# Optimization experiments

Measured on AMD Instinct MI355X. Metric: run time of the kernel, lower is better.

## Reference

```python
import jax, jax.numpy as jnp
import numpy as np

B, S, E, H = 4, 2048, 1024, 16
D = E // H  # key_size


def setup_inputs() -> dict:
    key = jax.random.key(0)
    ks = jax.random.split(key, 6)
    s = 1.0 / np.sqrt(E)
    return {
        "X": jax.random.normal(ks[0], (B, S, E), dtype=jnp.float32),
        "Wq": jax.random.uniform(ks[1], (E, E), jnp.float32, -s, s),
        "Wk": jax.random.uniform(ks[2], (E, E), jnp.float32, -s, s),
        "Wv": jax.random.uniform(ks[3], (E, E), jnp.float32, -s, s),
        "Wo": jax.random.uniform(ks[4], (E, E), jnp.float32, -s, s),
        "bo": jax.random.uniform(ks[5], (E,), jnp.float32, -s, s),
    }


def reference(X, Wq, Wk, Wv, Wo, bo):
    # Linear layers: y = x @ W^T (torch convention), no bias for q/k/v
    def split(x):  # [B,S,E] -> [B,H,S,D]
        return x.reshape(B, S, H, D).transpose(0, 2, 1, 3)

    q = split(X @ Wq.T)
    k = split(X @ Wk.T)
    v = split(X @ Wv.T)
    scale = jnp.asarray(np.sqrt(D), dtype=X.dtype)
    scores = jnp.einsum("bhqd,bhkd->bhqk", q, k) / scale
    probs = jax.nn.softmax(scores, axis=-1)
    ctx = jnp.einsum("bhqk,bhkd->bhqd", probs, v)
    out = ctx.transpose(0, 2, 1, 3).reshape(B, S, E)
    return out @ Wo.T + bo
```

## Files before the change

### kernel.cpp

```cpp
#include <hip/hip_runtime.h>
#include <hip/hip_bf16.h>

typedef short bf16x8 __attribute__((ext_vector_type(8)));
typedef float f32x4  __attribute__((ext_vector_type(4)));

__device__ __forceinline__ short f2bf(float f) {
    union { float f; unsigned u; } x; x.f = f;
    unsigned r = x.u + 0x7fffu + ((x.u >> 16) & 1u);
    return (short)(r >> 16);
}

__device__ __forceinline__ unsigned rbits(float f) {
    union { float f; unsigned u; } x; x.f = f;
    return x.u + 0x8000u;
}
__device__ __forceinline__ int pack2(float a, float b) {
    return (int)__builtin_amdgcn_perm(rbits(b), rbits(a), 0x07060302u);
}

__device__ __forceinline__ f32x4 mfma32k(bf16x8 a, bf16x8 b, f32x4 c) {
    return __builtin_amdgcn_mfma_f32_16x16x32_bf16(a, b, c, 0, 0, 0);
}

#define GLDS16(g, l)                                                            \
    __builtin_amdgcn_global_load_lds(                                           \
        (const __attribute__((address_space(1))) void*)(g),                     \
        (__attribute__((address_space(3))) void*)(l), 16, 0, 0)

static constexpr int Bb = 4, Ss = 2048, Ee = 1024, Hh = 16, Dd = 64;
static constexpr int Mrows = Bb * Ss;
static constexpr float CL2 = 0.1803368801111204f;

__global__ void cvt_all(const float* __restrict__ X,  const float* __restrict__ Wq,
                        const float* __restrict__ Wk, const float* __restrict__ Wv,
                        const float* __restrict__ Wo,
                        short* __restrict__ Xb, short* __restrict__ Wqk,
                        short* __restrict__ Wvb, short* __restrict__ Wob) {
    int bid = blockIdx.x;
    const float* src; short* dst; int off; float scale = 1.0f;
    if (bid < 8192) {
        src = X; dst = Xb; off = bid * 1024;
    } else {
        int wsel = (bid - 8192) >> 10;
        off = ((bid - 8192) & 1023) * 1024;
        if      (wsel == 0) { src = Wq; dst = Wqk;                scale = CL2; }
        else if (wsel == 1) { src = Wk; dst = Wqk + Ee * Ee; }
        else if (wsel == 2) { src = Wv; dst = Wvb; }
        else                { src = Wo; dst = Wob; }
    }
    int i = off + threadIdx.x * 4;
    float4 v = *(const float4*)(src + i);
    short4 o;
    o.x = f2bf(v.x * scale); o.y = f2bf(v.y * scale);
    o.z = f2bf(v.z * scale); o.w = f2bf(v.w * scale);
    *(short4*)(dst + i) = o;
}

__global__ __launch_bounds__(256, 3)
void gemm_fused(const short* __restrict__ A0, const short* __restrict__ B0,
                short* __restrict__ C0,
                const short* __restrict__ A1, const short* __restrict__ B1,
                short* __restrict__ C1, int split) {
    __shared__ __align__(16) short sA[128 * 32];
    __shared__ __align__(16) short sB[128 * 32];
    const int t = threadIdx.x, w = t >> 6, l = t & 63;
    const int lane16 = l & 15, quad = l >> 4;
    const int wm = (w >> 1) * 64, wn = (w & 1) * 64;

    int bid = blockIdx.x;
    const short *A, *Bm; short* C;
    int bm, bn, ldc; bool perm;
    if (bid < split) {
        bm = bid & 63; bn = bid >> 6;
        A = A0; Bm = B0; C = C0; ldc = 2048; perm = false;
    } else {
        int id = bid - split;
        bm = id & 7; bn = id >> 3;
        A = A1; Bm = B1; C = C1; ldc = 8192; perm = true;
    }

    f32x4 acc[4][4] = {};
    const short* Ab  = A  + (size_t)bm * 128 * 1024;
    const short* Bbp = Bm + (size_t)bn * 128 * 1024;
    const int s0 = w * 64 + l;
    const int ldsOff = (w * 64) * 8;

    for (int k0 = 0; k0 < 1024; k0 += 32) {
#pragma unroll
        for (int p = 0; p < 2; ++p) {
            int s = p * 256 + s0;
            int row = s >> 2, cs = s & 3;
            GLDS16(Ab + (size_t)row * 1024 + k0 + cs * 8, sA + p * 2048 + ldsOff);
            GLDS16(Bbp + (size_t)row * 1024 + k0 + cs * 8, sB + p * 2048 + ldsOff);
        }
        __syncthreads();
        bf16x8 af[4], bfr[4];
#pragma unroll
        for (int i = 0; i < 4; ++i) {
            af[i]  = *(const bf16x8*)(sA + (wm + i * 16 + lane16) * 32 + quad * 8);
            bfr[i] = *(const bf16x8*)(sB + (wn + i * 16 + lane16) * 32 + quad * 8);
        }
#pragma unroll
        for (int i = 0; i < 4; ++i)
#pragma unroll
            for (int j = 0; j < 4; ++j)
                acc[i][j] = mfma32k(af[i], bfr[j], acc[i][j]);
        __syncthreads();
    }

    const int sEven = (lane16 >> 2) * 8 + (lane16 & 3);
#pragma unroll
    for (int i = 0; i < 4; ++i)
#pragma unroll
        for (int j = 0; j < 4; ++j) {
            int row = bm * 128 + wm + i * 16 + quad * 4;
            int col = bn * 128 + wn + j * 16 + lane16;
            if (perm) col = (col & ~31) | (sEven + (j & 1) * 4);
#pragma unroll
            for (int r = 0; r < 4; ++r)
                C[(size_t)(row + r) * ldc + col] = f2bf(acc[i][j][r]);
        }
}

__global__ __launch_bounds__(256, 3)
void gemm_out(const short* __restrict__ A, const short* __restrict__ Bm,
              float* __restrict__ C, const float* __restrict__ bias) {
    __shared__ __align__(16) short sA[128 * 32];
    __shared__ __align__(16) short sB[128 * 32];
    const int t = threadIdx.x, w = t >> 6, l = t & 63;
    const int lane16 = l & 15, quad = l >> 4;
    const int wm = (w >> 1) * 64, wn = (w & 1) * 64;
    const int bm = blockIdx.x, bn = blockIdx.y;

    f32x4 acc[4][4] = {};
    const short* Ab  = A  + (size_t)bm * 128 * 1024;
    const short* Bbp = Bm + (size_t)bn * 128 * 1024;
    const int s0 = w * 64 + l;
    const int ldsOff = (w * 64) * 8;

    for (int k0 = 0; k0 < 1024; k0 += 32) {
#pragma unroll
        for (int p = 0; p < 2; ++p) {
            int s = p * 256 + s0;
            int row = s >> 2, cs = s & 3;
            GLDS16(Ab + (size_t)row * 1024 + k0 + cs * 8, sA + p * 2048 + ldsOff);
            GLDS16(Bbp + (size_t)row * 1024 + k0 + cs * 8, sB + p * 2048 + ldsOff);
        }
        __syncthreads();
        bf16x8 af[4], bfr[4];
#pragma unroll
        for (int i = 0; i < 4; ++i) {
            af[i]  = *(const bf16x8*)(sA + (wm + i * 16 + lane16) * 32 + quad * 8);
            bfr[i] = *(const bf16x8*)(sB + (wn + i * 16 + lane16) * 32 + quad * 8);
        }
#pragma unroll
        for (int i = 0; i < 4; ++i)
#pragma unroll
            for (int j = 0; j < 4; ++j)
                acc[i][j] = mfma32k(af[i], bfr[j], acc[i][j]);
        __syncthreads();
    }

#pragma unroll
    for (int i = 0; i < 4; ++i)
#pragma unroll
        for (int j = 0; j < 4; ++j) {
            int row = bm * 128 + wm + i * 16 + quad * 4;
            int col = bn * 128 + wn + j * 16 + lane16;
            float bv = bias[col];
#pragma unroll
            for (int r = 0; r < 4; ++r)
                C[(size_t)(row + r) * 1024 + col] = acc[i][j][r] + bv;
        }
}

__global__ __launch_bounds__(256, 4)
void attn_kernel(const short* __restrict__ QK, const short* __restrict__ VT,
                 short* __restrict__ CTX) {
    __shared__ __align__(16) short sK[8192];
    __shared__ __align__(16) short sV[8192];
    const int t = threadIdx.x, w = t >> 6, l = t & 63;
    const int lane16 = l & 15, quad = l >> 4;
    const int bh = blockIdx.x, qt = blockIdx.y;
    const int b = bh >> 4, h = bh & 15;

    const int qx8 = (quad ^ ((lane16 >> 1) & 3)) * 8;

    const short* Qb = QK + ((size_t)(b * 2048 + qt * 128)) * 2048 + h * 64;
    const short* Vb = VT + ((size_t)(h * 64)) * 8192 + (size_t)b * 2048;
    const int ldsOff = (w * 64) * 8;

    int off_kq[4], off_v[4];
#pragma unroll
    for (int p = 0; p < 4; ++p) {
        int c = p * 256 + t;
        int sw = ((c & 3) ^ ((c >> 3) & 3)) * 8;
        off_kq[p] = ((c >> 2) & 127) * 2048 + (c >> 9) * 32 + sw;
        off_v[p]  = ((c >> 2) & 63) * 8192 + (c >> 8) * 32 + sw;
    }

#pragma unroll
    for (int p = 0; p < 4; ++p)
        GLDS16(Qb + off_kq[p], sK + p * 2048 + ldsOff);
    __syncthreads();
    bf16x8 qf[2][2];
#pragma unroll
    for (int mt = 0; mt < 2; ++mt)
#pragma unroll
        for (int ks = 0; ks < 2; ++ks)
            qf[mt][ks] = *(const bf16x8*)(sK + ks * 4096 + (w * 32 + mt * 16 + lane16) * 32 + qx8);
    __syncthreads();

    const short one = (short)0x3F80;
    const bf16x8 ONE8 = {one, one, one, one, one, one, one, one};
    f32x4 lacc[2] = {};
    f32x4 o[2][4] = {};

    const short* kptr = QK + ((size_t)(b * 2048)) * 2048 + 1024 + h * 64;
    const short* vptr = Vb;

    auto QKB = [&](int a, f32x4 (&sc)[2][2]) {
        __builtin_amdgcn_s_setprio(1);
#pragma unroll
        for (int sub = 0; sub < 2; ++sub) {
            int nt = a * 2 + sub;
            bf16x8 kf0 = *(const bf16x8*)(sK + (nt * 16 + lane16) * 32 + qx8);
            bf16x8 kf1 = *(const bf16x8*)(sK + 4096 + (nt * 16 + lane16) * 32 + qx8);
#pragma unroll
            for (int mt = 0; mt < 2; ++mt) {
                f32x4 z = {};
                z = mfma32k(kf0, qf[mt][0], z);
                z = mfma32k(kf1, qf[mt][1], z);
                sc[mt][sub] = z;
            }
        }
        __builtin_amdgcn_s_setprio(0);
    };
    auto PVB = [&](int a, f32x4 (&sc)[2][2]) {
        bf16x8 pf[2];
#pragma unroll
        for (int mt = 0; mt < 2; ++mt) {
            union { int i[4]; bf16x8 v; } u;
#pragma unroll
            for (int sub = 0; sub < 2; ++sub) {
                f32x4 e;
#pragma unroll
                for (int r = 0; r < 4; ++r)
                    e[r] = __builtin_amdgcn_exp2f(sc[mt][sub][r]);
                u.i[sub * 2]     = pack2(e[0], e[1]);
                u.i[sub * 2 + 1] = pack2(e[2], e[3]);
            }
            pf[mt] = u.v;
        }
        __builtin_amdgcn_s_setprio(1);
#pragma unroll
        for (int mt = 0; mt < 2; ++mt)
            lacc[mt] = mfma32k(pf[mt], ONE8, lacc[mt]);
#pragma unroll
        for (int dt = 0; dt < 4; ++dt) {
            bf16x8 vf = *(const bf16x8*)(sV + a * 2048 + (dt * 16 + lane16) * 32 + qx8);
#pragma unroll
            for (int mt = 0; mt < 2; ++mt)
                o[mt][dt] = mfma32k(pf[mt], vf, o[mt][dt]);
        }
        __builtin_amdgcn_s_setprio(0);
    };

    for (int kt = 0; kt < 16; ++kt) {
#pragma unroll
        for (int p = 0; p < 4; ++p)
            GLDS16(kptr + off_kq[p], sK + p * 2048 + ldsOff);
#pragma unroll
        for (int p = 0; p < 4; ++p)
            GLDS16(vptr + off_v[p], sV + p * 2048 + ldsOff);
        kptr += (size_t)128 * 2048;
        vptr += 128;
        __syncthreads();

        f32x4 scA[2][2], scB[2][2];
        QKB(0, scA);
        QKB(1, scB);  PVB(0, scA);
        QKB(2, scA);  PVB(1, scB);
        QKB(3, scB);  PVB(2, scA);
                      PVB(3, scB);
        __syncthreads();
    }

#pragma unroll
    for (int mt = 0; mt < 2; ++mt)
#pragma unroll
        for (int r = 0; r < 4; ++r) {
            float inv = 1.0f / lacc[mt][r];
            int row = b * 2048 + qt * 128 + w * 32 + mt * 16 + quad * 4 + r;
#pragma unroll
            for (int dt = 0; dt < 4; ++dt)
                CTX[(size_t)row * 1024 + h * 64 + dt * 16 + lane16] = f2bf(o[mt][dt][r] * inv);
        }
}

extern "C" void kernel_launch(void* const* d_in, const int* in_sizes, int n_in,
                              void* d_out, int out_size, void* d_ws, size_t ws_size,
                              hipStream_t stream) {
    const float* X  = (const float*)d_in[0];
    const float* Wq = (const float*)d_in[1];
    const float* Wk = (const float*)d_in[2];
    const float* Wv = (const float*)d_in[3];
    const float* Wo = (const float*)d_in[4];
    const float* bo = (const float*)d_in[5];
    float* out = (float*)d_out;

    char* ws = (char*)d_ws;
    constexpr size_t OFF_XB  = 0;
    constexpr size_t OFF_WQK = OFF_XB  + (size_t)Mrows * Ee * 2;
    constexpr size_t OFF_WV  = OFF_WQK + (size_t)2 * Ee * Ee * 2;
    constexpr size_t OFF_WO  = OFF_WV  + (size_t)Ee * Ee * 2;
    constexpr size_t OFF_QK  = OFF_WO  + (size_t)Ee * Ee * 2;
    constexpr size_t OFF_VT  = OFF_QK  + (size_t)Mrows * 2048 * 2;
    constexpr size_t OFF_CTX = OFF_VT  + (size_t)Ee * Mrows * 2;
    short* Xb   = (short*)(ws + OFF_XB);
    short* Wqk  = (short*)(ws + OFF_WQK);
    short* Wvb  = (short*)(ws + OFF_WV);
    short* Wob  = (short*)(ws + OFF_WO);
    short* QKb  = (short*)(ws + OFF_QK);
    short* VTb  = (short*)(ws + OFF_VT);
    short* CTX  = (short*)(ws + OFF_CTX);

    cvt_all<<<12288, 256, 0, stream>>>(X, Wq, Wk, Wv, Wo, Xb, Wqk, Wvb, Wob);

    gemm_fused<<<1536, 256, 0, stream>>>(Xb, Wqk, QKb, Wvb, Xb, VTb, 1024);

    attn_kernel<<<dim3(Bb * Hh, Ss / 128), 256, 0, stream>>>(QKb, VTb, CTX);

    gemm_out<<<dim3(Mrows / 128, Ee / 128), 256, 0, stream>>>(CTX, Wob, out, bo);
}
```

Measured before the change: 256.5 us.

## Rewrite QKV projection GEMM with 256x256 tiles and double-buffered swizzled LDS

The fused Q/K/V projection GEMM now uses 512-thread blocks computing 256x256 output tiles with a K-step of 64, replacing 128x128 tiles with a K-step of 32. Global-to-LDS loads are double-buffered and interleaved with MFMA phases under s_setprio, and an XOR swizzle is applied to LDS to avoid bank conflicts. Block IDs are remapped across XCDs. The intent is more data reuse per block and better overlap of loads with compute, at the cost of 128 KB of LDS per block, higher register pressure and fewer blocks (384).

```diff
diff --git a/kernel.cpp b/kernel.cpp
--- a/kernel.cpp
+++ b/kernel.cpp
@@ -56,69 +56,121 @@
     *(short4*)(dst + i) = o;
 }
 
-__global__ __launch_bounds__(256, 3)
+__global__ __launch_bounds__(512, 2)
 void gemm_fused(const short* __restrict__ A0, const short* __restrict__ B0,
                 short* __restrict__ C0,
                 const short* __restrict__ A1, const short* __restrict__ B1,
-                short* __restrict__ C1, int split) {
-    __shared__ __align__(16) short sA[128 * 32];
-    __shared__ __align__(16) short sB[128 * 32];
-    const int t = threadIdx.x, w = t >> 6, l = t & 63;
+                short* __restrict__ C1) {
+    __shared__ __align__(16) short lds[65536];
+    const int t = threadIdx.x, l = t & 63, wv = t >> 6;
     const int lane16 = l & 15, quad = l >> 4;
-    const int wm = (w >> 1) * 64, wn = (w & 1) * 64;
+    const int wm = wv >> 2, wn = wv & 3;
 
     int bid = blockIdx.x;
+    int wg = (bid & 7) * 48 + (bid >> 3);
     const short *A, *Bm; short* C;
     int bm, bn, ldc; bool perm;
-    if (bid < split) {
-        bm = bid & 63; bn = bid >> 6;
-        A = A0; Bm = B0; C = C0; ldc = 2048; perm = false;
-    } else {
-        int id = bid - split;
-        bm = id & 7; bn = id >> 3;
-        A = A1; Bm = B1; C = C1; ldc = 8192; perm = true;
-    }
-
-    f32x4 acc[4][4] = {};
-    const short* Ab  = A  + (size_t)bm * 128 * 1024;
-    const short* Bbp = Bm + (size_t)bn * 128 * 1024;
-    const int s0 = w * 64 + l;
-    const int ldsOff = (w * 64) * 8;
-
-    for (int k0 = 0; k0 < 1024; k0 += 32) {
-#pragma unroll
-        for (int p = 0; p < 2; ++p) {
-            int s = p * 256 + s0;
-            int row = s >> 2, cs = s & 3;
-            GLDS16(Ab + (size_t)row * 1024 + k0 + cs * 8, sA + p * 2048 + ldsOff);
-            GLDS16(Bbp + (size_t)row * 1024 + k0 + cs * 8, sB + p * 2048 + ldsOff);
-        }
-        __syncthreads();
-        bf16x8 af[4], bfr[4];
-#pragma unroll
-        for (int i = 0; i < 4; ++i) {
-            af[i]  = *(const bf16x8*)(sA + (wm + i * 16 + lane16) * 32 + quad * 8);
-            bfr[i] = *(const bf16x8*)(sB + (wn + i * 16 + lane16) * 32 + quad * 8);
-        }
-#pragma unroll
-        for (int i = 0; i < 4; ++i)
-#pragma unroll
-            for (int j = 0; j < 4; ++j)
-                acc[i][j] = mfma32k(af[i], bfr[j], acc[i][j]);
-        __syncthreads();
-    }
+    if (wg < 256) { bm = wg & 31; bn = wg >> 5; A = A0; Bm = B0; C = C0; ldc = 2048; perm = false; }
+    else { int v = wg - 256; bm = v & 3; bn = v >> 2; A = A1; Bm = B1; C = C1; ldc = 8192; perm = true; }
+
+    const short* Ab = A  + (size_t)bm * 256 * 1024;
+    const short* Bp = Bm + (size_t)bn * 256 * 1024;
+
+    const int grow = t >> 3;
+    const int lsl  = ((t & 7) ^ ((t >> 3) & 7)) * 8;
+    const short* gA = Ab + (size_t)grow * 1024 + lsl;
+    const short* gB = Bp + (size_t)grow * 1024 + lsl;
+
+#define STAGE8(gsrc, matOff, half, j, T, buf)                                   \
+    GLDS16((gsrc) + ((half) * 128 + (j) * 64) * 1024 + (T) * 64,                \
+           lds + (buf) * 32768 + (matOff) + (half) * 8192 + (j) * 4096 + wv * 512)
+
+    const int fsw0 = ((quad)     ^ (lane16 & 7)) * 8;
+    const int fsw1 = ((quad + 4) ^ (lane16 & 7)) * 8;
+    const int aoff = (wm * 128 + lane16) * 64;
+    const int boff = (wn * 64  + lane16) * 64;
+
+    f32x4 acc[8][4] = {};
+
+    STAGE8(gA, 0,     0, 0, 0, 0); STAGE8(gA, 0,     0, 1, 0, 0);
+    STAGE8(gA, 0,     1, 0, 0, 0); STAGE8(gA, 0,     1, 1, 0, 0);
+    STAGE8(gB, 16384, 0, 0, 0, 0); STAGE8(gB, 16384, 0, 1, 0, 0);
+    STAGE8(gB, 16384, 1, 0, 0, 0); STAGE8(gB, 16384, 1, 1, 0, 0);
+    STAGE8(gA, 0,     0, 0, 1, 1); STAGE8(gA, 0,     0, 1, 1, 1);
+    asm volatile("s_waitcnt vmcnt(2)" ::: "memory");
+    __builtin_amdgcn_s_barrier();
+
+#define ARD(MI0)                                                                \
+    a0 = *(const bf16x8*)(sAc + aoff + (MI0) * 1024 + fsw0);                    \
+    a1 = *(const bf16x8*)(sAc + aoff + (MI0) * 1024 + fsw1);                    \
+    a2 = *(const bf16x8*)(sAc + aoff + ((MI0) + 1) * 1024 + fsw0);              \
+    a3 = *(const bf16x8*)(sAc + aoff + ((MI0) + 1) * 1024 + fsw1);
+
+#define MFQ(MI0)                                                                \
+    __builtin_amdgcn_s_setprio(1);                                              \
+    _Pragma("unroll")                                                           \
+    for (int nj = 0; nj < 4; ++nj) {                                            \
+        acc[MI0][nj]       = mfma32k(a0, bf[nj][0], acc[MI0][nj]);              \
+        acc[MI0][nj]       = mfma32k(a1, bf[nj][1], acc[MI0][nj]);              \
+        acc[(MI0) + 1][nj] = mfma32k(a2, bf[nj][0], acc[(MI0) + 1][nj]);        \
+        acc[(MI0) + 1][nj] = mfma32k(a3, bf[nj][1], acc[(MI0) + 1][nj]);        \
+    }                                                                           \
+    __builtin_amdgcn_s_setprio(0);
+
+    for (int T = 0; T < 16; ++T) {
+        const int cur = T & 1, nxt = cur ^ 1;
+        const short* sAc = lds + cur * 32768;
+        const short* sBc = sAc + 16384;
+        bf16x8 bf[4][2];
+#pragma unroll
+        for (int nj = 0; nj < 4; ++nj) {
+            bf[nj][0] = *(const bf16x8*)(sBc + boff + nj * 1024 + fsw0);
+            bf[nj][1] = *(const bf16x8*)(sBc + boff + nj * 1024 + fsw1);
+        }
+        bf16x8 a0, a1, a2, a3;
+        ARD(0)
+        if (T < 15) { STAGE8(gA, 0, 1, 0, T + 1, nxt); STAGE8(gA, 0, 1, 1, T + 1, nxt); }
+        __builtin_amdgcn_s_barrier();
+        MFQ(0)
+        __builtin_amdgcn_s_barrier();
+        ARD(2)
+        if (T < 15) { STAGE8(gB, 16384, 0, 0, T + 1, nxt); STAGE8(gB, 16384, 0, 1, T + 1, nxt); }
+        __builtin_amdgcn_s_barrier();
+        MFQ(2)
+        __builtin_amdgcn_s_barrier();
+        ARD(4)
+        if (T < 15) { STAGE8(gB, 16384, 1, 0, T + 1, nxt); STAGE8(gB, 16384, 1, 1, T + 1, nxt); }
+        __builtin_amdgcn_s_barrier();
+        MFQ(4)
+        __builtin_amdgcn_s_barrier();
+        ARD(6)
+        __builtin_amdgcn_s_barrier();
+        MFQ(6)
+        __builtin_amdgcn_s_barrier();
+        if (T < 14) {
+            STAGE8(gA, 0, 0, 0, T + 2, cur); STAGE8(gA, 0, 0, 1, T + 2, cur);
+            asm volatile("s_waitcnt vmcnt(2)" ::: "memory");
+            __builtin_amdgcn_s_barrier();
+        } else if (T == 14) {
+            asm volatile("s_waitcnt vmcnt(0)" ::: "memory");
+            __builtin_amdgcn_s_barrier();
+        }
+    }
+#undef ARD
+#undef MFQ
+#undef STAGE8
 
     const int sEven = (lane16 >> 2) * 8 + (lane16 & 3);
 #pragma unroll
-    for (int i = 0; i < 4; ++i)
-#pragma unroll
-        for (int j = 0; j < 4; ++j) {
-            int row = bm * 128 + wm + i * 16 + quad * 4;
-            int col = bn * 128 + wn + j * 16 + lane16;
-            if (perm) col = (col & ~31) | (sEven + (j & 1) * 4);
+    for (int mi = 0; mi < 8; ++mi)
+#pragma unroll
+        for (int nj = 0; nj < 4; ++nj) {
+            int row = bm * 256 + wm * 128 + mi * 16 + quad * 4;
+            int col = bn * 256 + wn * 64 + nj * 16 + lane16;
+            if (perm) col = (col & ~31) | (sEven + (nj & 1) * 4);
 #pragma unroll
             for (int r = 0; r < 4; ++r)
-                C[(size_t)(row + r) * ldc + col] = f2bf(acc[i][j][r]);
+                C[(size_t)(row + r) * ldc + col] = f2bf(acc[mi][nj][r]);
         }
 }
 
@@ -327,7 +379,7 @@
 
     cvt_all<<<12288, 256, 0, stream>>>(X, Wq, Wk, Wv, Wo, Xb, Wqk, Wvb, Wob);
 
-    gemm_fused<<<1536, 256, 0, stream>>>(Xb, Wqk, QKb, Wvb, Xb, VTb, 1024);
+    gemm_fused<<<384, 512, 0, stream>>>(Xb, Wqk, QKb, Wvb, Xb, VTb);
 
     attn_kernel<<<dim3(Bb * Hh, Ss / 128), 256, 0, stream>>>(QKb, VTb, CTX);
 
```

Result: no change. 252.4 us (-1.6%).
